# Kernel tuning notes

Measured on AMD Instinct MI355X. Metric: run time of the kernel, lower is better.

## Reference

```python
import jax, jax.numpy as jnp
import numpy as np

LAMBDA_TSA = 0.1
K = 25
P = 1
EPS = 1e-08


def setup_inputs() -> dict:
    key = jax.random.key(0)
    k1, k2, k3, k4 = jax.random.split(key, 4)
    B, D = 8192, 64
    return {
        "outputs": jax.random.normal(k1, (B, D), dtype=jnp.float32),
        "targets": jax.random.normal(k2, (B, D), dtype=jnp.float32),
        "latent": jax.random.normal(k3, (B, D), dtype=jnp.float32),
        "raw": jax.random.normal(k4, (B, D), dtype=jnp.float32),
    }


def _tsa_value(raw, latent):
    # raw, latent: [B, D]
    B, D = raw.shape
    # squared euclidean distances via gram trick (monotone in distance, so
    # topk-smallest indices match torch.cdist + topk(largest=False))
    sq = jnp.sum(raw * raw, axis=1)                      # [B]
    d2 = sq[:, None] + sq[None, :] - 2.0 * (raw @ raw.T)  # [B, B]
    _, idx = jax.lax.top_k(-d2, K + 1)                   # [B, K+1] nearest first
    nbrs = idx[:, 1:]                                    # [B, K] drop self

    Z = latent[nbrs]                                     # [B, K, D]
    X = raw[nbrs]                                        # [B, K, D]
    Zc = Z - jnp.mean(Z, axis=1, keepdims=True)
    Xc = X - jnp.mean(X, axis=1, keepdims=True)
    denom = K - 1 + EPS
    Cz = jnp.einsum('bkd,bke->bde', Zc, Zc) / denom       # [B, D, D]
    Cx = jnp.einsum('bkd,bke->bde', Xc, Xc) / denom       # [B, D, D]

    _, Uz = jnp.linalg.eigh(Cz)                          # ascending eigvals
    _, Ux = jnp.linalg.eigh(Cx)
    Ui = Uz[:, :, -P:]                                   # [B, D, P] top-P eigvecs
    Vi = Ux[:, :, -P:]
    Pz = jnp.einsum('bdp,bep->bde', Ui, Ui)              # projector [B, D, D]
    Px = jnp.einsum('bdp,bep->bde', Vi, Vi)
    per_sample = jnp.sum((Pz - Px) ** 2, axis=(1, 2))    # frobenius norm squared
    return jnp.mean(per_sample)


def reference(outputs, targets, latent, raw):
    recon = jnp.mean((outputs - targets) ** 2)
    # offload_cpu=True detaches raw/latent in the torch module
    raw_s = jax.lax.stop_gradient(raw)
    latent_s = jax.lax.stop_gradient(latent)
    tsa = LAMBDA_TSA * _tsa_value(raw_s, latent_s)
    return recon + tsa
```

## Files before the change

kernel.cpp:

```cpp
#include <hip/hip_runtime.h>
#include <hip/hip_bf16.h>


#define NB 8192
#define ND 64
#define KSEL 26
#define ROUNDS 8

__global__ __launch_bounds__(256) void tsa_prep_kernel(const float* __restrict__ raw,
                                                       const float* __restrict__ outputs,
                                                       const float* __restrict__ targets,
                                                       float* __restrict__ sq,
                                                       float* __restrict__ rawT,
                                                       float* __restrict__ reconP) {
    __shared__ float tile[64][65];
    const int bid = blockIdx.x;
    const int t = threadIdx.x;
    if (bid < 2048) {
        int row = bid * 4 + (t >> 6);
        int lane = t & 63;
        float v = raw[row * 64 + lane];
        float s = v * v;
        #pragma unroll
        for (int off = 1; off < 64; off <<= 1) s += __shfl_xor(s, off);
        if (lane == 0) sq[row] = s;
    } else if (bid < 2176) {
        int r0 = (bid - 2048) * 64;
        #pragma unroll
        for (int r = 0; r < 4; ++r) {
            int e = r * 256 + t;
            int m = e >> 4, c4 = e & 15;
            float4 v = ((const float4*)raw)[(r0 + m) * 16 + c4];
            tile[m][c4 * 4 + 0] = v.x; tile[m][c4 * 4 + 1] = v.y;
            tile[m][c4 * 4 + 2] = v.z; tile[m][c4 * 4 + 3] = v.w;
        }
        __syncthreads();
        #pragma unroll
        for (int r = 0; r < 4; ++r) {
            int e = r * 256 + t;
            int k = e >> 4, c4 = e & 15;
            float4 v;
            v.x = tile[c4 * 4 + 0][k]; v.y = tile[c4 * 4 + 1][k];
            v.z = tile[c4 * 4 + 2][k]; v.w = tile[c4 * 4 + 3][k];
            ((float4*)rawT)[k * 2048 + (r0 >> 2) + c4] = v;
        }
    } else {
        int idx = (bid - 2176) * 256 + t;
        float4 a = ((const float4*)outputs)[idx];
        float4 b = ((const float4*)targets)[idx];
        float dx = a.x - b.x, dy = a.y - b.y, dz = a.z - b.z, dw = a.w - b.w;
        float s = dx * dx + dy * dy + dz * dz + dw * dw;
        #pragma unroll
        for (int off = 1; off < 64; off <<= 1) s += __shfl_xor(s, off);
        __shared__ float ps[4];
        if ((t & 63) == 0) ps[t >> 6] = s;
        __syncthreads();
        if (t == 0) reconP[bid - 2176] = ps[0] + ps[1] + ps[2] + ps[3];
    }
}

__global__ __launch_bounds__(256) void tsa_dist_kernel(const float* __restrict__ rawT,
                                                       const float* __restrict__ sq,
                                                       float* __restrict__ d2,
                                                       int rowBase) {
    __shared__ float At[64 * 128];
    __shared__ float Bt[64 * 128];
    const int t = threadIdx.x;
    const int m0 = rowBase + blockIdx.y * 128;
    const int n0 = blockIdx.x * 128;
    const float4* rT4 = (const float4*)rawT;
    float4* At4 = (float4*)At;
    float4* Bt4 = (float4*)Bt;
    #pragma unroll
    for (int r = 0; r < 8; ++r) {
        int e = r * 256 + t;
        int k = e >> 5, c = e & 31;
        At4[e] = rT4[k * 2048 + (m0 >> 2) + c];
        Bt4[e] = rT4[k * 2048 + (n0 >> 2) + c];
    }
    __syncthreads();
    const int tx = t >> 4;
    const int ty = t & 15;
    float acc[8][8];
    #pragma unroll
    for (int i = 0; i < 8; ++i)
        #pragma unroll
        for (int j = 0; j < 8; ++j) acc[i][j] = 0.0f;

    #pragma unroll 4
    for (int k = 0; k < 64; ++k) {
        float4 a0 = At4[k * 32 + tx * 2 + 0];
        float4 a1 = At4[k * 32 + tx * 2 + 1];
        float4 b0 = Bt4[k * 32 + ty];
        float4 b1 = Bt4[k * 32 + 16 + ty];
        float av[8] = {a0.x, a0.y, a0.z, a0.w, a1.x, a1.y, a1.z, a1.w};
        float bw[8] = {b0.x, b0.y, b0.z, b0.w, b1.x, b1.y, b1.z, b1.w};
        #pragma unroll
        for (int i = 0; i < 8; ++i)
            #pragma unroll
            for (int j = 0; j < 8; ++j)
                acc[i][j] += av[i] * bw[j];
    }
    float sqm[8], sqn[8];
    #pragma unroll
    for (int i = 0; i < 8; ++i) sqm[i] = sq[m0 + tx * 8 + i];
    #pragma unroll
    for (int j = 0; j < 4; ++j) {
        sqn[j]     = sq[n0 + ty * 4 + j];
        sqn[4 + j] = sq[n0 + 64 + ty * 4 + j];
    }
    #pragma unroll
    for (int i = 0; i < 8; ++i) {
        size_t rowoff = (size_t)(m0 - rowBase + tx * 8 + i) * 8192;
        float4 w0, w1;
        w0.x = sqm[i] + sqn[0] - 2.0f * acc[i][0];
        w0.y = sqm[i] + sqn[1] - 2.0f * acc[i][1];
        w0.z = sqm[i] + sqn[2] - 2.0f * acc[i][2];
        w0.w = sqm[i] + sqn[3] - 2.0f * acc[i][3];
        w1.x = sqm[i] + sqn[4] - 2.0f * acc[i][4];
        w1.y = sqm[i] + sqn[5] - 2.0f * acc[i][5];
        w1.z = sqm[i] + sqn[6] - 2.0f * acc[i][6];
        w1.w = sqm[i] + sqn[7] - 2.0f * acc[i][7];
        float4* wp = (float4*)(d2 + rowoff + n0);
        wp[ty] = w0;
        wp[16 + ty] = w1;
    }
}

__global__ __launch_bounds__(256) void tsa_select_kernel(const float* __restrict__ d2,
                                                         int* __restrict__ nbrs,
                                                         int rowBase) {
    const int t = threadIdx.x;
    const int lane = t & 63;
    const int wv = t >> 6;
    const int i = rowBase + blockIdx.x;
    const float4* row4 = (const float4*)(d2 + (size_t)blockIdx.x * 8192u);

    float v[32];
    #pragma unroll
    for (int r = 0; r < 8; ++r) {
        float4 f = row4[wv * 512 + r * 64 + lane];
        v[4 * r + 0] = f.x; v[4 * r + 1] = f.y;
        v[4 * r + 2] = f.z; v[4 * r + 3] = f.w;
    }
    __shared__ float selV[4][KSEL];
    __shared__ int   selJ[4][KSEL];
    unsigned removed = 0;
    for (int round = 0; round < KSEL; ++round) {
        float bv = 3.0e38f; int bq = 0;
        #pragma unroll
        for (int q = 0; q < 32; ++q) {
            bool ok = ((removed >> q) & 1u) == 0u;
            bool c = ok && (v[q] < bv);
            bv = c ? v[q] : bv;
            bq = c ? q : bq;
        }
        int bj = wv * 2048 + (bq >> 2) * 256 + lane * 4 + (bq & 3);
        #pragma unroll
        for (int off = 1; off < 64; off <<= 1) {
            float rv = __shfl_xor(bv, off);
            int rj = __shfl_xor(bj, off);
            bool take = (rv < bv) || (rv == bv && rj < bj);
            bv = take ? rv : bv;
            bj = take ? rj : bj;
        }
        int jl = bj - wv * 2048;
        int ol = (jl >> 2) & 63;
        int oq = ((jl >> 8) << 2) | (jl & 3);
        if (lane == ol) removed |= (1u << oq);
        if (lane == 0) { selV[wv][round] = bv; selJ[wv][round] = bj; }
    }
    __syncthreads();
    if (wv == 0) {
        bool has = lane < 52;
        int p0 = lane, p1 = lane + 52;
        float v0 = has ? selV[p0 / KSEL][p0 % KSEL] : 3.0e38f;
        int   j0 = has ? selJ[p0 / KSEL][p0 % KSEL] : 0x7ffffffe;
        float v1 = has ? selV[p1 / KSEL][p1 % KSEL] : 3.0e38f;
        int   j1 = has ? selJ[p1 / KSEL][p1 % KSEL] : 0x7ffffffe;
        unsigned rm = 0;
        for (int round = 0; round < KSEL; ++round) {
            float bv = 3.0e38f; int bj = 0x7fffffff;
            if (!(rm & 1u)) { bv = v0; bj = j0; }
            if (!(rm & 2u) && (v1 < bv || (v1 == bv && j1 < bj))) { bv = v1; bj = j1; }
            #pragma unroll
            for (int off = 1; off < 64; off <<= 1) {
                float rv = __shfl_xor(bv, off);
                int rj = __shfl_xor(bj, off);
                bool take = (rv < bv) || (rv == bv && rj < bj);
                bv = take ? rv : bv;
                bj = take ? rj : bj;
            }
            if (bv == v0 && bj == j0) rm |= 1u;
            else if (bv == v1 && bj == j1) rm |= 2u;
            if (lane == 0 && round > 0) nbrs[i * 25 + round - 1] = bj;
        }
    }
}

__global__ __launch_bounds__(256) void tsa_eigen_kernel(const int* __restrict__ nbrs,
                                                        const float* __restrict__ latent,
                                                        const float* __restrict__ raw,
                                                        float* __restrict__ tsaV) {
    __shared__ __align__(16) float pool[8][1696];
    const int t = threadIdx.x, lane = t & 63, wv = t >> 6;
    const int i = blockIdx.x * 4 + wv;
    const int half = lane >> 5;
    const int b = lane & 31;
    const bool act = b < 25;
    const int bb = act ? b : 0;
    const float* src = half ? raw : latent;
    float* slice = pool[wv * 2 + half];

    int nb = 0;
    if (act) {
        nb = nbrs[i * 25 + b];
        const float4* s4 = (const float4*)(src + nb * 64);
        float4* dst = (float4*)(slice + b * 68);
        #pragma unroll
        for (int c = 0; c < 16; ++c) dst[c] = s4[c];
    }
    asm volatile("s_waitcnt lgkmcnt(0)" ::: "memory");

    float g[25];
    #pragma unroll
    for (int a = 0; a < 25; ++a) g[a] = 0.0f;
    #pragma unroll 1
    for (int ch = 0; ch < 4; ++ch) {
        float ow[16];
        const float4* op = (const float4*)(slice + bb * 68);
        ((float4*)ow)[0] = op[ch * 4 + 0];
        ((float4*)ow)[1] = op[ch * 4 + 1];
        ((float4*)ow)[2] = op[ch * 4 + 2];
        ((float4*)ow)[3] = op[ch * 4 + 3];
        #pragma unroll
        for (int a = 0; a < 25; ++a) {
            float rr[16];
            const float4* rp = (const float4*)(slice + a * 68);
            ((float4*)rr)[0] = rp[ch * 4 + 0];
            ((float4*)rr)[1] = rp[ch * 4 + 1];
            ((float4*)rr)[2] = rp[ch * 4 + 2];
            ((float4*)rr)[3] = rp[ch * 4 + 3];
            float s = 0.0f;
            #pragma unroll
            for (int d4 = 0; d4 < 16; ++d4) s += ow[d4] * rr[d4];
            g[a] += s;
        }
    }

    {
        float rs_own = 0.0f;
        #pragma unroll
        for (int a = 0; a < 25; ++a) rs_own += g[a];
        float grand = 0.0f;
        float rsA[25];
        #pragma unroll
        for (int a = 0; a < 25; ++a) {
            rsA[a] = __shfl(rs_own, half * 32 + a);
            grand += rsA[a];
        }
        const float c1 = 1.0f / 25.0f, c2 = 1.0f / 625.0f;
        #pragma unroll
        for (int a = 0; a < 25; ++a)
            g[a] = g[a] - rsA[a] * c1 - rs_own * c1 + grand * c2;
    }

    #pragma unroll 1
    for (int rd = 0; rd < ROUNDS; ++rd) {
        float ss = 0.0f;
        #pragma unroll
        for (int r2 = 0; r2 < 25; ++r2) ss += g[r2] * g[r2];
        ss = act ? ss : 0.0f;
        #pragma unroll
        for (int off = 1; off < 32; off <<= 1) ss += __shfl_xor(ss, off);
        float inv = 1.0f / ss;
        if (act) {
            float4* gw = (float4*)(slice + b * 28);
            gw[0] = make_float4(g[0], g[1], g[2], g[3]);
            gw[1] = make_float4(g[4], g[5], g[6], g[7]);
            gw[2] = make_float4(g[8], g[9], g[10], g[11]);
            gw[3] = make_float4(g[12], g[13], g[14], g[15]);
            gw[4] = make_float4(g[16], g[17], g[18], g[19]);
            gw[5] = make_float4(g[20], g[21], g[22], g[23]);
            gw[6] = make_float4(g[24], 0.0f, 0.0f, 0.0f);
        }
        asm volatile("s_waitcnt lgkmcnt(0)" ::: "memory");
        float ng[25];
        #pragma unroll
        for (int r2 = 0; r2 < 25; ++r2) ng[r2] = 0.0f;
        #pragma unroll
        for (int c = 0; c < 25; ++c) {
            float cc2[28];
            const float4* gr = (const float4*)(slice + c * 28);
            ((float4*)cc2)[0] = gr[0];
            ((float4*)cc2)[1] = gr[1];
            ((float4*)cc2)[2] = gr[2];
            ((float4*)cc2)[3] = gr[3];
            ((float4*)cc2)[4] = gr[4];
            ((float4*)cc2)[5] = gr[5];
            ((float4*)cc2)[6] = gr[6];
            float m2 = g[c];
            #pragma unroll
            for (int r2 = 0; r2 < 25; ++r2) ng[r2] += cc2[r2] * m2;
        }
        #pragma unroll
        for (int r2 = 0; r2 < 25; ++r2) g[r2] = ng[r2] * inv;
    }

    if (act) {
        float4* gw = (float4*)(slice + b * 28);
        gw[0] = make_float4(g[0], g[1], g[2], g[3]);
        gw[1] = make_float4(g[4], g[5], g[6], g[7]);
        gw[2] = make_float4(g[8], g[9], g[10], g[11]);
        gw[3] = make_float4(g[12], g[13], g[14], g[15]);
        gw[4] = make_float4(g[16], g[17], g[18], g[19]);
        gw[5] = make_float4(g[20], g[21], g[22], g[23]);
        gw[6] = make_float4(g[24], 0.0f, 0.0f, 0.0f);
    }
    asm volatile("s_waitcnt lgkmcnt(0)" ::: "memory");

    float dv = act ? slice[b * 28 + b] : -1.0f;
    int bi = b;
    #pragma unroll
    for (int off = 1; off < 32; off <<= 1) {
        float ov = __shfl_xor(dv, off);
        int oi = __shfl_xor(bi, off);
        bool take = (ov > dv) || (ov == dv && oi < bi);
        dv = take ? ov : dv;
        bi = take ? oi : bi;
    }
    int jz = __shfl(bi, 0);
    int jxm = __shfl(bi, 32);

    const float* slice0 = pool[wv * 2 + 0];
    const float* slice1 = pool[wv * 2 + 1];
    float wzArr[28], wxArr[28];
    {
        const float4* wz4 = (const float4*)(slice0 + jz * 28);
        const float4* wx4 = (const float4*)(slice1 + jxm * 28);
        #pragma unroll
        for (int q = 0; q < 7; ++q) {
            ((float4*)wzArr)[q] = wz4[q];
            ((float4*)wxArr)[q] = wx4[q];
        }
    }
    float szs = 0.0f, sxs = 0.0f;
    #pragma unroll
    for (int k = 0; k < 25; ++k) { szs += wzArr[k]; sxs += wxArr[k]; }
    float azc = szs * (1.0f / 25.0f), axc = sxs * (1.0f / 25.0f);

    float uz = 0.0f, ux = 0.0f;
    #pragma unroll
    for (int k = 0; k < 25; ++k) {
        int nbz = __shfl(nb, k);
        int nbx = __shfl(nb, 32 + k);
        uz += latent[nbz * 64 + lane] * (wzArr[k] - azc);
        ux += raw[nbx * 64 + lane] * (wxArr[k] - axc);
    }
    float aa = uz * uz, bbv = ux * ux, ccv = uz * ux;
    #pragma unroll
    for (int off = 1; off < 64; off <<= 1) {
        aa += __shfl_xor(aa, off);
        bbv += __shfl_xor(bbv, off);
        ccv += __shfl_xor(ccv, off);
    }
    if (lane == 0) {
        float dot2 = (ccv * ccv) / fmaxf(aa * bbv, 1e-30f);
        tsaV[i] = 2.0f - 2.0f * dot2;
    }
}

__global__ __launch_bounds__(256) void tsa_final_kernel(const float* __restrict__ tsaV,
                                                        const float* __restrict__ reconP,
                                                        float* __restrict__ out) {
    const int t = threadIdx.x;
    float s = 0.0f;
    const float4* v4 = (const float4*)tsaV;
    for (int e = t; e < 2048; e += 256) {
        float4 v = v4[e];
        s += (v.x + v.y) + (v.z + v.w);
    }
    float r = 0.0f;
    if (t < 128) {
        float4 p = ((const float4*)reconP)[t];
        r = (p.x + p.y) + (p.z + p.w);
    }
    #pragma unroll
    for (int off = 1; off < 64; off <<= 1) {
        s += __shfl_xor(s, off);
        r += __shfl_xor(r, off);
    }
    __shared__ float ps[4], pr[4];
    if ((t & 63) == 0) { ps[t >> 6] = s; pr[t >> 6] = r; }
    __syncthreads();
    if (t == 0) {
        float tot = ps[0] + ps[1] + ps[2] + ps[3];
        float rec = pr[0] + pr[1] + pr[2] + pr[3];
        out[0] = rec * (1.0f / 524288.0f) + 0.1f * (tot * (1.0f / 8192.0f));
    }
}

extern "C" void kernel_launch(void* const* d_in, const int* in_sizes, int n_in,
                              void* d_out, int out_size, void* d_ws, size_t ws_size,
                              hipStream_t stream) {
    const float* outputs = (const float*)d_in[0];
    const float* targets = (const float*)d_in[1];
    const float* latent  = (const float*)d_in[2];
    const float* raw     = (const float*)d_in[3];

    float* ws = (float*)d_ws;
    float* sq     = ws;
    float* rawT   = ws + 8192;
    int*   nbrs   = (int*)(ws + 532480);
    float* reconP = ws + 737280;
    float* tsaV   = ws + 737792;
    float* d2buf  = ws + 745984;

    size_t availF = ws_size / 4;
    int R = 2048;
    while (R > 128 && (size_t)745984 + (size_t)R * 8192 > availF) R >>= 1;

    tsa_prep_kernel<<<2688, 256, 0, stream>>>(raw, outputs, targets, sq, rawT, reconP);

    for (int rb = 0; rb < 8192; rb += R) {
        dim3 g(64, R / 128);
        tsa_dist_kernel<<<g, 256, 0, stream>>>(rawT, sq, d2buf, rb);
        tsa_select_kernel<<<R, 256, 0, stream>>>(d2buf, nbrs, rb);
    }
    tsa_eigen_kernel<<<2048, 256, 0, stream>>>(nbrs, latent, raw, tsaV);
    tsa_final_kernel<<<1, 256, 0, stream>>>(tsaV, reconP, (float*)d_out);
}
```

Before: 710.8 us.

## Replace full-row top-k with threshold filter from first column chunk

Measured after the change: 703.0 us. Within noise of the previous version (-1.1%).

```diff
diff --git a/kernel.cpp b/kernel.cpp
--- a/kernel.cpp
+++ b/kernel.cpp
@@ -6,6 +6,15 @@
 #define ND 64
 #define KSEL 26
 #define ROUNDS 8
+#define W0 2048
+#define NCH 12
+#define CCAP 32
+
+#define FINF 3.0e38f
+
+__device__ __forceinline__ bool lexless(float v, int j, float v2, int j2) {
+    return (v < v2) || (v == v2 && j < j2);
+}
 
 __global__ __launch_bounds__(256) void tsa_prep_kernel(const float* __restrict__ raw,
                                                        const float* __restrict__ outputs,
@@ -59,10 +68,10 @@
     }
 }
 
-__global__ __launch_bounds__(256) void tsa_dist_kernel(const float* __restrict__ rawT,
-                                                       const float* __restrict__ sq,
-                                                       float* __restrict__ d2,
-                                                       int rowBase) {
+__global__ __launch_bounds__(256) void tsa_dist0_kernel(const float* __restrict__ rawT,
+                                                        const float* __restrict__ sq,
+                                                        float* __restrict__ d2,
+                                                        int rowBase) {
     __shared__ float At[64 * 128];
     __shared__ float Bt[64 * 128];
     const int t = threadIdx.x;
@@ -111,7 +120,7 @@
     }
     #pragma unroll
     for (int i = 0; i < 8; ++i) {
-        size_t rowoff = (size_t)(m0 - rowBase + tx * 8 + i) * 8192;
+        size_t rowoff = (size_t)(m0 - rowBase + tx * 8 + i) * W0;
         float4 w0, w1;
         w0.x = sqm[i] + sqn[0] - 2.0f * acc[i][0];
         w0.y = sqm[i] + sqn[1] - 2.0f * acc[i][1];
@@ -127,27 +136,27 @@
     }
 }
 
-__global__ __launch_bounds__(256) void tsa_select_kernel(const float* __restrict__ d2,
-                                                         int* __restrict__ nbrs,
-                                                         int rowBase) {
+__global__ __launch_bounds__(256) void tsa_sel0_kernel(const float* __restrict__ d2,
+                                                       float* __restrict__ sel26V,
+                                                       int* __restrict__ sel26J,
+                                                       int rowBase) {
     const int t = threadIdx.x;
     const int lane = t & 63;
     const int wv = t >> 6;
-    const int i = rowBase + blockIdx.x;
-    const float4* row4 = (const float4*)(d2 + (size_t)blockIdx.x * 8192u);
+    const int lrow = blockIdx.x * 4 + wv;
+    const int i = rowBase + lrow;
+    const float4* row4 = (const float4*)(d2 + (size_t)lrow * W0);
 
     float v[32];
     #pragma unroll
     for (int r = 0; r < 8; ++r) {
-        float4 f = row4[wv * 512 + r * 64 + lane];
+        float4 f = row4[r * 64 + lane];
         v[4 * r + 0] = f.x; v[4 * r + 1] = f.y;
         v[4 * r + 2] = f.z; v[4 * r + 3] = f.w;
     }
-    __shared__ float selV[4][KSEL];
-    __shared__ int   selJ[4][KSEL];
     unsigned removed = 0;
     for (int round = 0; round < KSEL; ++round) {
-        float bv = 3.0e38f; int bq = 0;
+        float bv = FINF; int bq = 0;
         #pragma unroll
         for (int q = 0; q < 32; ++q) {
             bool ok = ((removed >> q) & 1u) == 0u;
@@ -155,7 +164,7 @@
             bv = c ? v[q] : bv;
             bq = c ? q : bq;
         }
-        int bj = wv * 2048 + (bq >> 2) * 256 + lane * 4 + (bq & 3);
+        int bj = (bq >> 2) * 256 + lane * 4 + (bq & 3);
         #pragma unroll
         for (int off = 1; off < 64; off <<= 1) {
             float rv = __shfl_xor(bv, off);
@@ -164,37 +173,192 @@
             bv = take ? rv : bv;
             bj = take ? rj : bj;
         }
-        int jl = bj - wv * 2048;
-        int ol = (jl >> 2) & 63;
-        int oq = ((jl >> 8) << 2) | (jl & 3);
+        int ol = (bj >> 2) & 63;
+        int oq = ((bj >> 8) << 2) | (bj & 3);
         if (lane == ol) removed |= (1u << oq);
-        if (lane == 0) { selV[wv][round] = bv; selJ[wv][round] = bj; }
+        if (lane == 0) { sel26V[i * KSEL + round] = bv; sel26J[i * KSEL + round] = bj; }
+    }
+}
+
+__global__ __launch_bounds__(256) void tsa_filter_kernel(const float* __restrict__ rawT,
+                                                         const float* __restrict__ sq,
+                                                         const float* __restrict__ sel26V,
+                                                         const int* __restrict__ sel26J,
+                                                         float* __restrict__ survV,
+                                                         int* __restrict__ survJ,
+                                                         int* __restrict__ cnt) {
+    __shared__ float At[64 * 128];
+    __shared__ float Bt[64 * 128];
+    const int t = threadIdx.x;
+    const int ch = blockIdx.x;
+    const int m0 = blockIdx.y * 128;
+    const int c0 = W0 + ch * 512;
+    const float4* rT4 = (const float4*)rawT;
+    float4* At4 = (float4*)At;
+    float4* Bt4 = (float4*)Bt;
+
+    #pragma unroll
+    for (int r = 0; r < 8; ++r) {
+        int e = r * 256 + t;
+        int k = e >> 5, c = e & 31;
+        At4[e] = rT4[k * 2048 + (m0 >> 2) + c];
+        Bt4[e] = rT4[k * 2048 + (c0 >> 2) + c];
     }
     __syncthreads();
-    if (wv == 0) {
-        bool has = lane < 52;
-        int p0 = lane, p1 = lane + 52;
-        float v0 = has ? selV[p0 / KSEL][p0 % KSEL] : 3.0e38f;
-        int   j0 = has ? selJ[p0 / KSEL][p0 % KSEL] : 0x7ffffffe;
-        float v1 = has ? selV[p1 / KSEL][p1 % KSEL] : 3.0e38f;
-        int   j1 = has ? selJ[p1 / KSEL][p1 % KSEL] : 0x7ffffffe;
-        unsigned rm = 0;
-        for (int round = 0; round < KSEL; ++round) {
-            float bv = 3.0e38f; int bj = 0x7fffffff;
-            if (!(rm & 1u)) { bv = v0; bj = j0; }
-            if (!(rm & 2u) && (v1 < bv || (v1 == bv && j1 < bj))) { bv = v1; bj = j1; }
-            #pragma unroll
-            for (int off = 1; off < 64; off <<= 1) {
-                float rv = __shfl_xor(bv, off);
-                int rj = __shfl_xor(bj, off);
-                bool take = (rv < bv) || (rv == bv && rj < bj);
-                bv = take ? rv : bv;
-                bj = take ? rj : bj;
+
+    const int tx = t >> 4;
+    const int ty = t & 15;
+    const int grp = (t & 63) >> 4;
+    float sqm[8], Tv[8]; int Tj[8]; int cntr[8];
+    #pragma unroll
+    for (int i = 0; i < 8; ++i) {
+        int row = m0 + tx * 8 + i;
+        sqm[i] = sq[row];
+        Tv[i] = sel26V[row * KSEL + 25];
+        Tj[i] = sel26J[row * KSEL + 25];
+        cntr[i] = 0;
+    }
+
+    #pragma unroll 1
+    for (int tile = 0; tile < 4; ++tile) {
+        const int n0 = c0 + tile * 128;
+        float4 pre[8];
+        if (tile < 3) {
+            int nn0 = n0 + 128;
+            #pragma unroll
+            for (int r = 0; r < 8; ++r) {
+                int e = r * 256 + t;
+                int k = e >> 5, c = e & 31;
+                pre[r] = rT4[k * 2048 + (nn0 >> 2) + c];
             }
-            if (bv == v0 && bj == j0) rm |= 1u;
-            else if (bv == v1 && bj == j1) rm |= 2u;
-            if (lane == 0 && round > 0) nbrs[i * 25 + round - 1] = bj;
-        }
+        }
+        float acc[8][8];
+        #pragma unroll
+        for (int i = 0; i < 8; ++i)
+            #pragma unroll
+            for (int j = 0; j < 8; ++j) acc[i][j] = 0.0f;
+        #pragma unroll 4
+        for (int k = 0; k < 64; ++k) {
+            float4 a0 = At4[k * 32 + tx * 2 + 0];
+            float4 a1 = At4[k * 32 + tx * 2 + 1];
+            float4 b0 = Bt4[k * 32 + ty];
+            float4 b1 = Bt4[k * 32 + 16 + ty];
+            float av[8] = {a0.x, a0.y, a0.z, a0.w, a1.x, a1.y, a1.z, a1.w};
+            float bw[8] = {b0.x, b0.y, b0.z, b0.w, b1.x, b1.y, b1.z, b1.w};
+            #pragma unroll
+            for (int i = 0; i < 8; ++i)
+                #pragma unroll
+                for (int j = 0; j < 8; ++j)
+                    acc[i][j] += av[i] * bw[j];
+        }
+        float sqn[8];
+        #pragma unroll
+        for (int j = 0; j < 4; ++j) {
+            sqn[j]     = sq[n0 + ty * 4 + j];
+            sqn[4 + j] = sq[n0 + 64 + ty * 4 + j];
+        }
+        #pragma unroll 1
+        for (int i = 0; i < 8; ++i) {
+            const int row = m0 + tx * 8 + i;
+            float v[8]; int jx[8];
+            bool any = false;
+            #pragma unroll
+            for (int j = 0; j < 8; ++j) {
+                v[j] = sqm[i] + sqn[j] - 2.0f * acc[i][j];
+                jx[j] = n0 + ((j < 4) ? (ty * 4 + j) : (64 + ty * 4 + j - 4));
+                any = any || lexless(v[j], jx[j], Tv[i], Tj[i]);
+            }
+            unsigned long long bal = __ballot(any);
+            unsigned m16 = (unsigned)((bal >> (grp * 16)) & 0xFFFFull);
+            if (m16) {
+                int base = cntr[i];
+                #pragma unroll 1
+                for (int j = 0; j < 8; ++j) {
+                    bool p = lexless(v[j], jx[j], Tv[i], Tj[i]);
+                    unsigned long long bj2 = __ballot(p);
+                    unsigned pm = (unsigned)((bj2 >> (grp * 16)) & 0xFFFFull);
+                    if (p) {
+                        int off = base + __popc(pm & ((1u << ty) - 1u));
+                        if (off < CCAP) {
+                            int sidx = (row * NCH + ch) * CCAP + off;
+                            survV[sidx] = v[j];
+                            survJ[sidx] = jx[j];
+                        }
+                    }
+                    base += __popc(pm);
+                }
+                cntr[i] = base;
+            }
+        }
+        if (tile < 3) {
+            __syncthreads();
+            #pragma unroll
+            for (int r = 0; r < 8; ++r) Bt4[r * 256 + t] = pre[r];
+            __syncthreads();
+        }
+    }
+    if (ty == 0) {
+        #pragma unroll
+        for (int i = 0; i < 8; ++i) {
+            int row = m0 + tx * 8 + i;
+            cnt[row * NCH + ch] = (cntr[i] < CCAP) ? cntr[i] : CCAP;
+        }
+    }
+}
+
+__global__ __launch_bounds__(256) void tsa_merge_kernel(const float* __restrict__ sel26V,
+                                                        const int* __restrict__ sel26J,
+                                                        const float* __restrict__ survV,
+                                                        const int* __restrict__ survJ,
+                                                        const int* __restrict__ cnt,
+                                                        int* __restrict__ nbrs) {
+    const int t = threadIdx.x, lane = t & 63, wv = t >> 6;
+    const int row = blockIdx.x * 4 + wv;
+    int pfx[NCH + 1];
+    pfx[0] = KSEL;
+    #pragma unroll
+    for (int c = 0; c < NCH; ++c) {
+        int cc = cnt[row * NCH + c];
+        cc = (cc < CCAP) ? cc : CCAP;
+        pfx[c + 1] = pfx[c] + cc;
+    }
+    const int total = pfx[NCH];
+    float m[7]; int mj[7];
+    #pragma unroll 1
+    for (int s = 0; s < 7; ++s) {
+        int e = lane + s * 64;
+        float val = FINF; int jj = 0x7f000000 + e;
+        if (e < KSEL) {
+            val = sel26V[row * KSEL + e];
+            jj = sel26J[row * KSEL + e];
+        } else if (e < total) {
+            int c = 0;
+            #pragma unroll
+            for (int q = 0; q < NCH; ++q)
+                if (e >= pfx[q + 1]) c = q + 1;
+            int off = e - pfx[c];
+            val = survV[(row * NCH + c) * CCAP + off];
+            jj = survJ[(row * NCH + c) * CCAP + off];
+        }
+        m[s] = val; mj[s] = jj;
+    }
+    unsigned rem = 0;
+    for (int round = 0; round < KSEL; ++round) {
+        float bv = FINF; int bj = 0x7fffffff; int bq = -1;
+        #pragma unroll
+        for (int s = 0; s < 7; ++s) {
+            bool ok = ((rem >> s) & 1u) == 0u;
+            if (ok && lexless(m[s], mj[s], bv, bj)) { bv = m[s]; bj = mj[s]; bq = s; }
+        }
+        float obv = bv; int obj = bj;
+        #pragma unroll
+        for (int off = 1; off < 64; off <<= 1) {
+            float rv = __shfl_xor(bv, off);
+            int rj = __shfl_xor(bj, off);
+            if (lexless(rv, rj, bv, bj)) { bv = rv; bj = rj; }
+        }
+        if (bq >= 0 && obv == bv && obj == bj) rem |= 1u << bq;
+        if (lane == 0 && round > 0) nbrs[row * 25 + round - 1] = bj;
     }
 }
 
@@ -414,19 +578,29 @@
     int*   nbrs   = (int*)(ws + 532480);
     float* reconP = ws + 737280;
     float* tsaV   = ws + 737792;
-    float* d2buf  = ws + 745984;
+    float* sel26V = ws + 745984;
+    int*   sel26J = (int*)(ws + 958976);
+    int*   cnt    = (int*)(ws + 1171968);
+    float* survV  = ws + 1270272;
+    int*   survJ  = (int*)(ws + 4416000);
+    float* d2_0   = ws + 7561728;
 
     size_t availF = ws_size / 4;
-    int R = 2048;
-    while (R > 128 && (size_t)745984 + (size_t)R * 8192 > availF) R >>= 1;
+    int RB = 8192;
+    while (RB > 1024 && (size_t)7561728 + (size_t)RB * W0 > availF) RB >>= 1;
 
     tsa_prep_kernel<<<2688, 256, 0, stream>>>(raw, outputs, targets, sq, rawT, reconP);
 
-    for (int rb = 0; rb < 8192; rb += R) {
-        dim3 g(64, R / 128);
-        tsa_dist_kernel<<<g, 256, 0, stream>>>(rawT, sq, d2buf, rb);
-        tsa_select_kernel<<<R, 256, 0, stream>>>(d2buf, nbrs, rb);
-    }
+    for (int rb = 0; rb < 8192; rb += RB) {
+        dim3 g(W0 / 128, RB / 128);
+        tsa_dist0_kernel<<<g, 256, 0, stream>>>(rawT, sq, d2_0, rb);
+        tsa_sel0_kernel<<<RB / 4, 256, 0, stream>>>(d2_0, sel26V, sel26J, rb);
+    }
+    {
+        dim3 g(NCH, 64);
+        tsa_filter_kernel<<<g, 256, 0, stream>>>(rawT, sq, sel26V, sel26J, survV, survJ, cnt);
+    }
+    tsa_merge_kernel<<<2048, 256, 0, stream>>>(sel26V, sel26J, survV, survJ, cnt, nbrs);
     tsa_eigen_kernel<<<2048, 256, 0, stream>>>(nbrs, latent, raw, tsaV);
     tsa_final_kernel<<<1, 256, 0, stream>>>(tsaV, reconP, (float*)d_out);
 }
```
